# Performance work log

Hardware: AMD Instinct MI355X
Metric: run time of the kernel (lower is better)

## Reference

```python
import jax, jax.numpy as jnp
import numpy as np

B, T, C = 32, 1024, 512
D = C // 2          # reduction_factor_input = 2 -> conv1d(1x1) filters = 256
U = 256             # LSTM units
O = U // 1          # reduction_factor_output = 1 -> 256


def setup_inputs() -> dict:
    key = jax.random.key(0)
    ks = jax.random.split(key, 8)
    s = lambda *d: 1.0 / np.sqrt(d[0])
    return {
        "x": jax.random.normal(ks[0], (B, T, C), jnp.float32),
        "w_in": jax.random.normal(ks[1], (C, D), jnp.float32) * s(C),
        "b_in": jnp.zeros((D,), jnp.float32),
        "kernel": jax.random.normal(ks[2], (D, 4 * U), jnp.float32) * s(D),
        "rec_kernel": jax.random.normal(ks[3], (U, 4 * U), jnp.float32) * s(U),
        "bias": jnp.zeros((4 * U,), jnp.float32),
        "w_out": jax.random.normal(ks[4], (U, O), jnp.float32) * s(U),
        "b_out": jnp.zeros((O,), jnp.float32),
    }


def _lstm(xz, rec_kernel):
    # xz: [T, B, 4U] precomputed input projection (x @ kernel + bias)
    def step(carry, xt):
        h, c = carry
        z = xt + h @ rec_kernel  # [B, 4U]
        i, f, g, o = jnp.split(z, 4, axis=-1)  # Keras gate order: i, f, c, o
        i = jax.nn.sigmoid(i)
        f = jax.nn.sigmoid(f)
        g = jnp.tanh(g)
        o = jax.nn.sigmoid(o)
        c = f * c + i * g
        h = o * jnp.tanh(c)
        return (h, c), h

    b = xz.shape[1]
    init = (jnp.zeros((b, U), xz.dtype), jnp.zeros((b, U), xz.dtype))
    _, hs = jax.lax.scan(step, init, xz)
    return hs  # [T, B, U]


def reference(x, w_in, b_in, kernel, rec_kernel, bias, w_out, b_out):
    # Conv1D kernel_size=1 == per-timestep dense projection
    xin = x @ w_in + b_in                      # [B, T, D]
    xz = xin @ kernel + bias                   # [B, T, 4U]
    hs = _lstm(jnp.transpose(xz, (1, 0, 2)), rec_kernel)  # [T, B, U]
    hs = jnp.transpose(hs, (1, 0, 2))          # [B, T, U]
    return hs @ w_out + b_out                  # [B, T, O]
```

## Files before the change

### kernel.cpp

```cpp
#include <hip/hip_runtime.h>


#define DEV static __device__ __forceinline__

typedef __attribute__((ext_vector_type(8))) short short8;
typedef __attribute__((ext_vector_type(4))) float floatx4;
typedef _Float16 half8 __attribute__((ext_vector_type(8)));

static constexpr int Bsz = 32, T = 1024, C = 512, D = 256, U = 256, FU = 1024;
static constexpr int M = Bsz * T;

DEV float bfu2f(unsigned int u) { union { unsigned int i; float f; } v; v.i = u; return v.f; }
DEV float bf2f(unsigned short u) { return bfu2f(((unsigned int)u) << 16); }
DEV unsigned short f2bf(float f) {
    union { float f; unsigned int i; } v; v.f = f;
    return (unsigned short)((v.i + 0x7fffu + ((v.i >> 16) & 1u)) >> 16);
}
DEV float sigmf(float x) { return 1.0f / (1.0f + __expf(-x)); }
DEV float tanhfast(float x) {
    const float a = __expf(-2.0f * fabsf(x));
    const float t = (1.0f - a) / (1.0f + a);
    return copysignf(t, x);
}
DEV half8 h8c(uint4 v) { return __builtin_bit_cast(half8, v); }

DEV short ld_bf(const float* p) { return (short)f2bf(*p); }
DEV short ld_bf(const unsigned short* p) { return (short)*p; }
DEV short8 ld_frag(const unsigned short* p) { return *(const short8*)p; }
DEV short8 ld_frag(const float* p) {
    short8 v;
#pragma unroll
    for (int j = 0; j < 8; j++) v[j] = (short)f2bf(p[j]);
    return v;
}
DEV float ldxz1(const float* p) { return *p; }
DEV float ldxz1(const unsigned short* p) { return bf2f(*p); }

template <int K, int N, int MT, int NS, bool OUTF32, typename AT, typename BT>
__global__ __launch_bounds__(64) void gemm_mfma(
    const AT* __restrict__ A,
    const BT* __restrict__ Bm,
    const float* __restrict__ bias,
    void* __restrict__ Cv)
{
    constexpr int KC = K / 32;
    const int lane = threadIdx.x;
    const int quad = lane >> 4, lr = lane & 15;
    constexpr int NSG = N / (16 * NS);
    const int sg = blockIdx.x % NSG;
    const int mb = blockIdx.x / NSG;
    const int n0 = sg * 16 * NS;

    short8 bf[NS][KC];
    float biasv[NS];
#pragma unroll
    for (int s = 0; s < NS; s++) {
        const int n = n0 + s * 16 + lr;
        biasv[s] = bias[n];
#pragma unroll
        for (int kc = 0; kc < KC; kc++) {
            short8 v;
#pragma unroll
            for (int j = 0; j < 8; j++) {
                const int k = kc * 32 + quad * 8 + j;
                v[j] = ld_bf(&Bm[(size_t)k * N + n]);
            }
            bf[s][kc] = v;
        }
    }

    for (int mt = 0; mt < MT; mt++) {
        const int m0 = (mb * MT + mt) * 16;
        const AT* Ap = A + (size_t)(m0 + lr) * K + quad * 8;
        floatx4 acc[NS];
#pragma unroll
        for (int s = 0; s < NS; s++) acc[s] = (floatx4){0.f, 0.f, 0.f, 0.f};
#pragma unroll
        for (int kc = 0; kc < KC; kc++) {
            short8 af = ld_frag(Ap + kc * 32);
#pragma unroll
            for (int s = 0; s < NS; s++)
                acc[s] = __builtin_amdgcn_mfma_f32_16x16x32_bf16(af, bf[s][kc], acc[s], 0, 0, 0);
        }
#pragma unroll
        for (int s = 0; s < NS; s++) {
            const int n = n0 + s * 16 + lr;
#pragma unroll
            for (int r = 0; r < 4; r++) {
                const int m = m0 + quad * 4 + r;
                const float val = acc[s][r] + biasv[s];
                if (OUTF32)
                    ((float*)Cv)[(size_t)m * N + n] = val;
                else
                    ((unsigned short*)Cv)[(size_t)m * N + n] = f2bf(val);
            }
        }
    }
}

__global__ __launch_bounds__(256) void pack_rec_mfma(const float* __restrict__ rec,
                                                     uint4* __restrict__ Pm)
{
    const int idx = blockIdx.x * 256 + threadIdx.x;
    const int lane = idx & 63;
    const int kc = (idx >> 6) & 7;
    const int strip = idx >> 9;
    const int q = lane >> 4, lr = lane & 15;
    const int col = strip * 16 + lr;
    const int k0 = kc * 32 + q * 8;
    union { unsigned short u[8]; uint4 v; } out;
#pragma unroll
    for (int j = 0; j < 8; j++) {
        const _Float16 h = (_Float16)rec[(size_t)(k0 + j) * FU + col];
        out.u[j] = __builtin_bit_cast(unsigned short, h);
    }
    Pm[idx] = out.v;
}

template <typename XZT>
__global__ __attribute__((amdgpu_flat_work_group_size(512, 512),
                          amdgpu_waves_per_eu(2, 2)))
void lstm_mfma(
    const XZT* __restrict__ xz,
    const uint4* __restrict__ Pm,
    unsigned short* __restrict__ hs)
{
    const int b = blockIdx.x;
    const int tid = threadIdx.x;
    const int w = tid >> 6;
    const int lane = tid & 63;
    const int q = lane >> 4, lr = lane & 15;

    __shared__ uint4 Wl[16 * 8 * 64];
    __shared__ __align__(16) unsigned short hbuf[2][U];

    for (int i = tid; i < 16 * 8 * 64; i += 512)
        Wl[i] = Pm[48 * 8 * 64 + i];
    if (tid < U) { hbuf[0][tid] = 0; hbuf[1][tid] = 0; }

    uint4 Wr[6][8];
#pragma unroll
    for (int s = 0; s < 6; s++) {
        const int strip = (s >> 1) * 16 + 2 * w + (s & 1);
#pragma unroll
        for (int kc = 0; kc < 8; kc++)
            Wr[s][kc] = Pm[(strip * 8 + kc) * 64 + lane];
    }
#pragma unroll
    for (int s = 0; s < 6; s++)
#pragma unroll
        for (int kc = 0; kc < 8; kc++)
            asm volatile("" : "+v"(Wr[s][kc].x), "+v"(Wr[s][kc].y),
                             "+v"(Wr[s][kc].z), "+v"(Wr[s][kc].w));
    __syncthreads();

    const XZT* xzb = xz + (size_t)b * T * FU;
    unsigned short* hsb = hs + (size_t)b * T * U;
    const int u0 = 32 * w + lr;

    float c0 = 0.f, c1 = 0.f;
    float xc[8], xn[8];
#pragma unroll
    for (int i = 0; i < 8; i++) { xc[i] = 0.f; xn[i] = 0.f; }
    if (q == 0) {
#pragma unroll
        for (int g2 = 0; g2 < 4; g2++) {
            xc[2 * g2]     = ldxz1(xzb + g2 * 256 + u0);
            xc[2 * g2 + 1] = ldxz1(xzb + g2 * 256 + u0 + 16);
        }
    }

    const uint4 z4 = {0u, 0u, 0u, 0u};
    uint4 afc = z4, afn = z4;

    for (int t = 0; t < T; t++) {
        const unsigned short* hb = hbuf[t & 1];
        unsigned short* hn = hbuf[(t + 1) & 1];

        const XZT* xzt1 = xzb + (size_t)(t + 1 < T ? t + 1 : t) * FU;
        if (q == 0) {
#pragma unroll
            for (int g2 = 0; g2 < 4; g2++) {
                xn[2 * g2]     = ldxz1(xzt1 + g2 * 256 + u0);
                xn[2 * g2 + 1] = ldxz1(xzt1 + g2 * 256 + u0 + 16);
            }
        }

        {
            floatx4 acc_i = {0.f,0.f,0.f,0.f}, acc_f = {0.f,0.f,0.f,0.f};
            floatx4 acc_g = {0.f,0.f,0.f,0.f}, acc_o = {0.f,0.f,0.f,0.f};
            if (lr == 0) afc = *(const uint4*)(hb + q * 8);
            uint4 stc = Wl[(2 * w * 8) * 64 + lane], stn = z4;
#pragma unroll
            for (int kc = 0; kc < 8; kc++) {
                if (kc < 7) {
                    if (lr == 0) afn = *(const uint4*)(hb + (kc + 1) * 32 + q * 8);
                    stn = Wl[(2 * w * 8 + kc + 1) * 64 + lane];
                }
                acc_i = __builtin_amdgcn_mfma_f32_16x16x32_f16(h8c(afc), h8c(Wr[0][kc]), acc_i, 0, 0, 0);
                acc_f = __builtin_amdgcn_mfma_f32_16x16x32_f16(h8c(afc), h8c(Wr[2][kc]), acc_f, 0, 0, 0);
                acc_g = __builtin_amdgcn_mfma_f32_16x16x32_f16(h8c(afc), h8c(Wr[4][kc]), acc_g, 0, 0, 0);
                acc_o = __builtin_amdgcn_mfma_f32_16x16x32_f16(h8c(afc), h8c(stc),       acc_o, 0, 0, 0);
                afc = afn; stc = stn;
            }
            const float zi = acc_i[0] + xc[0];
            const float zf = acc_f[0] + xc[2];
            const float zg = acc_g[0] + xc[4];
            const float zo = acc_o[0] + xc[6];
            const float iv = sigmf(zi), fv = sigmf(zf);
            const float gv = tanhfast(zg), ov = sigmf(zo);
            c0 = fv * c0 + iv * gv;
            const float hv = ov * tanhfast(c0);
            if (q == 0) {
                hn[u0] = __builtin_bit_cast(unsigned short, (_Float16)hv);
                hsb[(size_t)t * U + u0] = f2bf(hv);
            }
        }

        {
            floatx4 acc_i = {0.f,0.f,0.f,0.f}, acc_f = {0.f,0.f,0.f,0.f};
            floatx4 acc_g = {0.f,0.f,0.f,0.f}, acc_o = {0.f,0.f,0.f,0.f};
            if (lr == 0) afc = *(const uint4*)(hb + q * 8);
            uint4 stc = Wl[((2 * w + 1) * 8) * 64 + lane], stn = z4;
#pragma unroll
            for (int kc = 0; kc < 8; kc++) {
                if (kc < 7) {
                    if (lr == 0) afn = *(const uint4*)(hb + (kc + 1) * 32 + q * 8);
                    stn = Wl[((2 * w + 1) * 8 + kc + 1) * 64 + lane];
                }
                acc_i = __builtin_amdgcn_mfma_f32_16x16x32_f16(h8c(afc), h8c(Wr[1][kc]), acc_i, 0, 0, 0);
                acc_f = __builtin_amdgcn_mfma_f32_16x16x32_f16(h8c(afc), h8c(Wr[3][kc]), acc_f, 0, 0, 0);
                acc_g = __builtin_amdgcn_mfma_f32_16x16x32_f16(h8c(afc), h8c(Wr[5][kc]), acc_g, 0, 0, 0);
                acc_o = __builtin_amdgcn_mfma_f32_16x16x32_f16(h8c(afc), h8c(stc),       acc_o, 0, 0, 0);
                afc = afn; stc = stn;
            }
            const float zi = acc_i[0] + xc[1];
            const float zf = acc_f[0] + xc[3];
            const float zg = acc_g[0] + xc[5];
            const float zo = acc_o[0] + xc[7];
            const float iv = sigmf(zi), fv = sigmf(zf);
            const float gv = tanhfast(zg), ov = sigmf(zo);
            c1 = fv * c1 + iv * gv;
            const float hv = ov * tanhfast(c1);
            if (q == 0) {
                hn[u0 + 16] = __builtin_bit_cast(unsigned short, (_Float16)hv);
                hsb[(size_t)t * U + u0 + 16] = f2bf(hv);
            }
        }

#pragma unroll
        for (int i = 0; i < 8; i++) xc[i] = xn[i];
        __syncthreads();
    }
}

extern "C" void kernel_launch(void* const* d_in, const int* in_sizes, int n_in,
                              void* d_out, int out_size, void* d_ws, size_t ws_size,
                              hipStream_t stream)
{
    const float* x    = (const float*)d_in[0];
    const float* w_in = (const float*)d_in[1];
    const float* b_in = (const float*)d_in[2];
    const float* kern = (const float*)d_in[3];
    const float* rec  = (const float*)d_in[4];
    const float* bias = (const float*)d_in[5];
    const float* wout = (const float*)d_in[6];
    const float* bout = (const float*)d_in[7];

    char* ws = (char*)d_ws;
    const size_t rec_bytes = (size_t)64 * 8 * 64 * 16;
    const size_t xin_bytes = (size_t)M * D * 2;
    const size_t hs_bytes  = (size_t)M * U * 2;
    const size_t xz32_bytes = (size_t)M * FU * 4;
    const size_t base = rec_bytes + xin_bytes + hs_bytes;

    uint4* P = (uint4*)ws;
    unsigned short* xin_bf = (unsigned short*)(ws + rec_bytes);
    unsigned short* hs_bf  = (unsigned short*)(ws + rec_bytes + xin_bytes);
    char* xz_raw = ws + base;

    const bool use_f32 = ws_size >= base + xz32_bytes;

    pack_rec_mfma<<<128, 256, 0, stream>>>(rec, P);

    gemm_mfma<512, 256, 16, 2, false><<<(256 / 32) * (M / 256), 64, 0, stream>>>(
        x, w_in, b_in, (void*)xin_bf);

    if (use_f32) {
        float* xz = (float*)xz_raw;
        gemm_mfma<256, 1024, 16, 2, true><<<(1024 / 32) * (M / 256), 64, 0, stream>>>(
            xin_bf, kern, bias, (void*)xz);
        lstm_mfma<float><<<Bsz, 512, 0, stream>>>(xz, P, hs_bf);
    } else {
        unsigned short* xz = (unsigned short*)xz_raw;
        gemm_mfma<256, 1024, 16, 2, false><<<(1024 / 32) * (M / 256), 64, 0, stream>>>(
            xin_bf, kern, bias, (void*)xz);
        lstm_mfma<unsigned short><<<Bsz, 512, 0, stream>>>(xz, P, hs_bf);
    }

    gemm_mfma<256, 256, 16, 2, true><<<(256 / 32) * (M / 256), 64, 0, stream>>>(
        hs_bf, wout, bout, d_out);
}
```

Before: 2.156 ms.

## Restructure LSTM recurrence to 4 waves with shared-memory gate exchange

The recurrent LSTM kernel moves from 8 waves to 4 waves per batch element. Each wave now holds 12 weight strips in registers and reads 4 from LDS, computing full 16-column gate tiles that it writes to a shared z buffer. A second phase lets each thread own one hidden unit, applying the gate nonlinearities and writing h. The single double-buffered barrier per step becomes two lightweight barriers per step (raw s_barrier with an lgkm wait). This trades more MFMA work per wave and an extra LDS round trip for fewer waves and a simpler elementwise phase. The added risk is a longer serial critical path per timestep.

```diff
diff --git a/kernel.cpp b/kernel.cpp
--- a/kernel.cpp
+++ b/kernel.cpp
@@ -35,6 +35,8 @@
 }
 DEV float ldxz1(const float* p) { return *p; }
 DEV float ldxz1(const unsigned short* p) { return bf2f(*p); }
+
+#define BAR() asm volatile("s_waitcnt lgkmcnt(0)\n\ts_barrier" ::: "memory")
 
 template <int K, int N, int MT, int NS, bool OUTF32, typename AT, typename BT>
 __global__ __launch_bounds__(64) void gemm_mfma(
@@ -118,9 +120,9 @@
 }
 
 template <typename XZT>
-__global__ __attribute__((amdgpu_flat_work_group_size(512, 512),
-                          amdgpu_waves_per_eu(2, 2)))
-void lstm_mfma(
+__global__ __attribute__((amdgpu_flat_work_group_size(256, 256),
+                          amdgpu_waves_per_eu(1, 1)))
+void lstm_mfma4(
     const XZT* __restrict__ xz,
     const uint4* __restrict__ Pm,
     unsigned short* __restrict__ hs)
@@ -130,24 +132,27 @@
     const int w = tid >> 6;
     const int lane = tid & 63;
     const int q = lane >> 4, lr = lane & 15;
-
-    __shared__ uint4 Wl[16 * 8 * 64];
-    __shared__ __align__(16) unsigned short hbuf[2][U];
-
-    for (int i = tid; i < 16 * 8 * 64; i += 512)
-        Wl[i] = Pm[48 * 8 * 64 + i];
-    if (tid < U) { hbuf[0][tid] = 0; hbuf[1][tid] = 0; }
-
-    uint4 Wr[6][8];
-#pragma unroll
-    for (int s = 0; s < 6; s++) {
-        const int strip = (s >> 1) * 16 + 2 * w + (s & 1);
+    const int u = tid;
+
+    __shared__ uint4 Wls[16 * 8 * 64];
+    __shared__ float zsh[FU];
+    __shared__ __align__(16) unsigned short h_pk[U];
+
+    for (int i = tid; i < 16 * 8 * 64; i += 256) {
+        const int slot = i >> 9;
+        const int gs = 16 * (slot >> 2) + 12 + (slot & 3);
+        Wls[i] = Pm[(size_t)gs * 512 + (i & 511)];
+    }
+    if (tid < 128) ((unsigned int*)h_pk)[tid] = 0;
+
+    uint4 Wr[12][8];
+#pragma unroll
+    for (int s = 0; s < 12; s++)
 #pragma unroll
         for (int kc = 0; kc < 8; kc++)
-            Wr[s][kc] = Pm[(strip * 8 + kc) * 64 + lane];
-    }
-#pragma unroll
-    for (int s = 0; s < 6; s++)
+            Wr[s][kc] = Pm[((size_t)(16 * w + s) * 8 + kc) * 64 + lane];
+#pragma unroll
+    for (int s = 0; s < 12; s++)
 #pragma unroll
         for (int kc = 0; kc < 8; kc++)
             asm volatile("" : "+v"(Wr[s][kc].x), "+v"(Wr[s][kc].y),
@@ -156,101 +161,74 @@
 
     const XZT* xzb = xz + (size_t)b * T * FU;
     unsigned short* hsb = hs + (size_t)b * T * U;
-    const int u0 = 32 * w + lr;
-
-    float c0 = 0.f, c1 = 0.f;
-    float xc[8], xn[8];
-#pragma unroll
-    for (int i = 0; i < 8; i++) { xc[i] = 0.f; xn[i] = 0.f; }
-    if (q == 0) {
-#pragma unroll
-        for (int g2 = 0; g2 < 4; g2++) {
-            xc[2 * g2]     = ldxz1(xzb + g2 * 256 + u0);
-            xc[2 * g2 + 1] = ldxz1(xzb + g2 * 256 + u0 + 16);
-        }
-    }
-
-    const uint4 z4 = {0u, 0u, 0u, 0u};
-    uint4 afc = z4, afn = z4;
+    const char* hp = (const char*)h_pk;
+
+    float cst = 0.f;
+    float xzi = ldxz1(xzb + u),       xzf = ldxz1(xzb + 256 + u);
+    float xzg = ldxz1(xzb + 512 + u), xzo = ldxz1(xzb + 768 + u);
 
     for (int t = 0; t < T; t++) {
-        const unsigned short* hb = hbuf[t & 1];
-        unsigned short* hn = hbuf[(t + 1) & 1];
-
-        const XZT* xzt1 = xzb + (size_t)(t + 1 < T ? t + 1 : t) * FU;
-        if (q == 0) {
-#pragma unroll
-            for (int g2 = 0; g2 < 4; g2++) {
-                xn[2 * g2]     = ldxz1(xzt1 + g2 * 256 + u0);
-                xn[2 * g2 + 1] = ldxz1(xzt1 + g2 * 256 + u0 + 16);
-            }
-        }
-
+        float xzi_n = 0.f, xzf_n = 0.f, xzg_n = 0.f, xzo_n = 0.f;
+        if (t + 1 < T) {
+            const XZT* xt = xzb + (size_t)(t + 1) * FU;
+            xzi_n = ldxz1(xt + u);       xzf_n = ldxz1(xt + 256 + u);
+            xzg_n = ldxz1(xt + 512 + u); xzo_n = ldxz1(xt + 768 + u);
+        }
+
+#pragma unroll
+        for (int g = 0; g < 3; g++) {
+            floatx4 ac0 = {0.f,0.f,0.f,0.f}, ac1 = {0.f,0.f,0.f,0.f};
+            floatx4 ac2 = {0.f,0.f,0.f,0.f}, ac3 = {0.f,0.f,0.f,0.f};
+#pragma unroll
+            for (int kc = 0; kc < 8; kc++) {
+                const uint4 af = *(const uint4*)(hp + kc * 64 + q * 16);
+                ac0 = __builtin_amdgcn_mfma_f32_16x16x32_f16(h8c(af), h8c(Wr[g * 4 + 0][kc]), ac0, 0, 0, 0);
+                ac1 = __builtin_amdgcn_mfma_f32_16x16x32_f16(h8c(af), h8c(Wr[g * 4 + 1][kc]), ac1, 0, 0, 0);
+                ac2 = __builtin_amdgcn_mfma_f32_16x16x32_f16(h8c(af), h8c(Wr[g * 4 + 2][kc]), ac2, 0, 0, 0);
+                ac3 = __builtin_amdgcn_mfma_f32_16x16x32_f16(h8c(af), h8c(Wr[g * 4 + 3][kc]), ac3, 0, 0, 0);
+            }
+            if (q == 0) {
+                zsh[(16 * w + g * 4 + 0) * 16 + lr] = ac0[0];
+                zsh[(16 * w + g * 4 + 1) * 16 + lr] = ac1[0];
+                zsh[(16 * w + g * 4 + 2) * 16 + lr] = ac2[0];
+                zsh[(16 * w + g * 4 + 3) * 16 + lr] = ac3[0];
+            }
+        }
         {
-            floatx4 acc_i = {0.f,0.f,0.f,0.f}, acc_f = {0.f,0.f,0.f,0.f};
-            floatx4 acc_g = {0.f,0.f,0.f,0.f}, acc_o = {0.f,0.f,0.f,0.f};
-            if (lr == 0) afc = *(const uint4*)(hb + q * 8);
-            uint4 stc = Wl[(2 * w * 8) * 64 + lane], stn = z4;
+            floatx4 ac0 = {0.f,0.f,0.f,0.f}, ac1 = {0.f,0.f,0.f,0.f};
+            floatx4 ac2 = {0.f,0.f,0.f,0.f}, ac3 = {0.f,0.f,0.f,0.f};
 #pragma unroll
             for (int kc = 0; kc < 8; kc++) {
-                if (kc < 7) {
-                    if (lr == 0) afn = *(const uint4*)(hb + (kc + 1) * 32 + q * 8);
-                    stn = Wl[(2 * w * 8 + kc + 1) * 64 + lane];
-                }
-                acc_i = __builtin_amdgcn_mfma_f32_16x16x32_f16(h8c(afc), h8c(Wr[0][kc]), acc_i, 0, 0, 0);
-                acc_f = __builtin_amdgcn_mfma_f32_16x16x32_f16(h8c(afc), h8c(Wr[2][kc]), acc_f, 0, 0, 0);
-                acc_g = __builtin_amdgcn_mfma_f32_16x16x32_f16(h8c(afc), h8c(Wr[4][kc]), acc_g, 0, 0, 0);
-                acc_o = __builtin_amdgcn_mfma_f32_16x16x32_f16(h8c(afc), h8c(stc),       acc_o, 0, 0, 0);
-                afc = afn; stc = stn;
-            }
-            const float zi = acc_i[0] + xc[0];
-            const float zf = acc_f[0] + xc[2];
-            const float zg = acc_g[0] + xc[4];
-            const float zo = acc_o[0] + xc[6];
-            const float iv = sigmf(zi), fv = sigmf(zf);
-            const float gv = tanhfast(zg), ov = sigmf(zo);
-            c0 = fv * c0 + iv * gv;
-            const float hv = ov * tanhfast(c0);
+                const uint4 af = *(const uint4*)(hp + kc * 64 + q * 16);
+                const uint4 w0 = Wls[((w * 4 + 0) * 8 + kc) * 64 + lane];
+                const uint4 w1 = Wls[((w * 4 + 1) * 8 + kc) * 64 + lane];
+                const uint4 w2 = Wls[((w * 4 + 2) * 8 + kc) * 64 + lane];
+                const uint4 w3 = Wls[((w * 4 + 3) * 8 + kc) * 64 + lane];
+                ac0 = __builtin_amdgcn_mfma_f32_16x16x32_f16(h8c(af), h8c(w0), ac0, 0, 0, 0);
+                ac1 = __builtin_amdgcn_mfma_f32_16x16x32_f16(h8c(af), h8c(w1), ac1, 0, 0, 0);
+                ac2 = __builtin_amdgcn_mfma_f32_16x16x32_f16(h8c(af), h8c(w2), ac2, 0, 0, 0);
+                ac3 = __builtin_amdgcn_mfma_f32_16x16x32_f16(h8c(af), h8c(w3), ac3, 0, 0, 0);
+            }
             if (q == 0) {
-                hn[u0] = __builtin_bit_cast(unsigned short, (_Float16)hv);
-                hsb[(size_t)t * U + u0] = f2bf(hv);
-            }
-        }
-
-        {
-            floatx4 acc_i = {0.f,0.f,0.f,0.f}, acc_f = {0.f,0.f,0.f,0.f};
-            floatx4 acc_g = {0.f,0.f,0.f,0.f}, acc_o = {0.f,0.f,0.f,0.f};
-            if (lr == 0) afc = *(const uint4*)(hb + q * 8);
-            uint4 stc = Wl[((2 * w + 1) * 8) * 64 + lane], stn = z4;
-#pragma unroll
-            for (int kc = 0; kc < 8; kc++) {
-                if (kc < 7) {
-                    if (lr == 0) afn = *(const uint4*)(hb + (kc + 1) * 32 + q * 8);
-                    stn = Wl[((2 * w + 1) * 8 + kc + 1) * 64 + lane];
-                }
-                acc_i = __builtin_amdgcn_mfma_f32_16x16x32_f16(h8c(afc), h8c(Wr[1][kc]), acc_i, 0, 0, 0);
-                acc_f = __builtin_amdgcn_mfma_f32_16x16x32_f16(h8c(afc), h8c(Wr[3][kc]), acc_f, 0, 0, 0);
-                acc_g = __builtin_amdgcn_mfma_f32_16x16x32_f16(h8c(afc), h8c(Wr[5][kc]), acc_g, 0, 0, 0);
-                acc_o = __builtin_amdgcn_mfma_f32_16x16x32_f16(h8c(afc), h8c(stc),       acc_o, 0, 0, 0);
-                afc = afn; stc = stn;
-            }
-            const float zi = acc_i[0] + xc[1];
-            const float zf = acc_f[0] + xc[3];
-            const float zg = acc_g[0] + xc[5];
-            const float zo = acc_o[0] + xc[7];
-            const float iv = sigmf(zi), fv = sigmf(zf);
-            const float gv = tanhfast(zg), ov = sigmf(zo);
-            c1 = fv * c1 + iv * gv;
-            const float hv = ov * tanhfast(c1);
-            if (q == 0) {
-                hn[u0 + 16] = __builtin_bit_cast(unsigned short, (_Float16)hv);
-                hsb[(size_t)t * U + u0 + 16] = f2bf(hv);
-            }
-        }
-
-#pragma unroll
-        for (int i = 0; i < 8; i++) xc[i] = xn[i];
-        __syncthreads();
+                zsh[(16 * w + 12) * 16 + lr] = ac0[0];
+                zsh[(16 * w + 13) * 16 + lr] = ac1[0];
+                zsh[(16 * w + 14) * 16 + lr] = ac2[0];
+                zsh[(16 * w + 15) * 16 + lr] = ac3[0];
+            }
+        }
+        BAR();
+
+        const float iv = sigmf(zsh[u] + xzi);
+        const float fv = sigmf(zsh[u + 256] + xzf);
+        const float gv = tanhfast(zsh[u + 512] + xzg);
+        const float ov = sigmf(zsh[u + 768] + xzo);
+        cst = fv * cst + iv * gv;
+        const float hv = ov * tanhfast(cst);
+        h_pk[u] = __builtin_bit_cast(unsigned short, (_Float16)hv);
+        hsb[(size_t)t * U + u] = f2bf(hv);
+        BAR();
+
+        xzi = xzi_n; xzf = xzf_n; xzg = xzg_n; xzo = xzo_n;
     }
 }
 
@@ -274,28 +252,28 @@
     const size_t xz32_bytes = (size_t)M * FU * 4;
     const size_t base = rec_bytes + xin_bytes + hs_bytes;
 
-    uint4* P = (uint4*)ws;
+    uint4* Pm = (uint4*)ws;
     unsigned short* xin_bf = (unsigned short*)(ws + rec_bytes);
     unsigned short* hs_bf  = (unsigned short*)(ws + rec_bytes + xin_bytes);
     char* xz_raw = ws + base;
 
     const bool use_f32 = ws_size >= base + xz32_bytes;
 
-    pack_rec_mfma<<<128, 256, 0, stream>>>(rec, P);
+    pack_rec_mfma<<<128, 256, 0, stream>>>(rec, Pm);
 
     gemm_mfma<512, 256, 16, 2, false><<<(256 / 32) * (M / 256), 64, 0, stream>>>(
         x, w_in, b_in, (void*)xin_bf);
 
     if (use_f32) {
-        float* xz = (float*)xz_raw;
+        float* xzp = (float*)xz_raw;
         gemm_mfma<256, 1024, 16, 2, true><<<(1024 / 32) * (M / 256), 64, 0, stream>>>(
-            xin_bf, kern, bias, (void*)xz);
-        lstm_mfma<float><<<Bsz, 512, 0, stream>>>(xz, P, hs_bf);
+            xin_bf, kern, bias, (void*)xzp);
+        lstm_mfma4<float><<<Bsz, 256, 0, stream>>>(xzp, Pm, hs_bf);
     } else {
-        unsigned short* xz = (unsigned short*)xz_raw;
+        unsigned short* xzp = (unsigned short*)xz_raw;
         gemm_mfma<256, 1024, 16, 2, false><<<(1024 / 32) * (M / 256), 64, 0, stream>>>(
-            xin_bf, kern, bias, (void*)xz);
-        lstm_mfma<unsigned short><<<Bsz, 512, 0, stream>>>(xz, P, hs_bf);
+            xin_bf, kern, bias, (void*)xzp);
+        lstm_mfma4<unsigned short><<<Bsz, 256, 0, stream>>>(xzp, Pm, hs_bf);
     }
 
     gemm_mfma<256, 256, 16, 2, true><<<(256 / 32) * (M / 256), 64, 0, stream>>>(
```

After: 2.834 ms. 31.4% more time.
